# Kernel tuning notes

Measured on AMD Instinct MI355X. Metric: run time of the kernel, lower is better.

The kernel has to match this reference:

```python
import jax, jax.numpy as jnp
import numpy as np

CHAN = 128
IN_CHAN = 3
NB_OUT = 10
K = 2  # maxPoolKer


def affine_grid(theta, H, W):
    # theta: [C,2,3] -> grid [C,H,W,2], torch F.affine_grid align_corners=False
    xs = (2.0 * jnp.arange(W, dtype=jnp.float32) + 1.0) / W - 1.0
    ys = (2.0 * jnp.arange(H, dtype=jnp.float32) + 1.0) / H - 1.0
    gx, gy = jnp.meshgrid(xs, ys)  # [H,W]
    base = jnp.stack([gx, gy, jnp.ones_like(gx)], axis=-1)  # [H,W,3]
    return jnp.einsum('crk,hwk->chwr', theta, base)  # [...,0]=x, [...,1]=y


def grid_sample(img, grid):
    # img [M,H,W], grid [M,H,W,2]; bilinear, zeros padding, align_corners=False
    M, H, W = img.shape
    ix = ((grid[..., 0] + 1.0) * W - 1.0) * 0.5
    iy = ((grid[..., 1] + 1.0) * H - 1.0) * 0.5
    x0 = jnp.floor(ix)
    y0 = jnp.floor(iy)
    wx = ix - x0
    wy = iy - y0

    def tap(xi, yi):
        valid = (xi >= 0) & (xi <= W - 1) & (yi >= 0) & (yi <= H - 1)
        xc = jnp.clip(xi, 0, W - 1).astype(jnp.int32)
        yc = jnp.clip(yi, 0, H - 1).astype(jnp.int32)
        v = jax.vmap(lambda im, y, x: im[y, x])(img, yc, xc)
        return jnp.where(valid, v, 0.0)

    v00 = tap(x0, y0)
    v01 = tap(x0 + 1.0, y0)
    v10 = tap(x0, y0 + 1.0)
    v11 = tap(x0 + 1.0, y0 + 1.0)
    return (1.0 - wy) * ((1.0 - wx) * v00 + wx * v01) + wy * ((1.0 - wx) * v10 + wx * v11)


def geom_layer(x, geo, lin, box):
    # x [B,Ci,H,W]; lin [C,Ci]; geo,box [C,2,3]
    B, Ci, H, W = x.shape
    C = lin.shape[0]
    y = jnp.einsum('ci,bihw->bchw', lin, x)  # channel linear combine
    grid = affine_grid(geo, H, W)            # [C,H,W,2], shared across batch
    samp = jax.vmap(lambda yb: grid_sample(yb, grid))(y)  # [B,C,H,W]
    bgrid = affine_grid(box, H, W)
    boxm = grid_sample(jnp.ones((C, H, W), samp.dtype), bgrid)  # BoxPool mask
    return samp * boxm[None]


def maxpool_g(x, k):
    # MaxPool2d_G: depthwise box-filter conv -> argmax -> gather window from padded x
    B, C, H, W = x.shape
    ch, cw = H // k, W // k
    ker = jnp.ones((1, 1, ch, cw), x.dtype) / (ch + cw)
    xr = x.reshape(B * C, 1, H, W)
    conv = jax.lax.conv_general_dilated(
        xr, ker, (1, 1), [(ch // 2, ch // 2), (cw // 2, cw // 2)])
    conv = conv[:, :, :H, :W].reshape(B, C, H * W)
    argm = jnp.argmax(conv, axis=-1)
    r = argm // H  # original code uses origImgSize[0]; assumes square H==W
    c = argm % W
    padH, padW = H + H // k, W + W // k
    top = padH // 2 - H // 2
    left = padW // 2 - W // 2
    padded = jnp.zeros((B, C, padH, padW), x.dtype).at[:, :, top:top + H, left:left + W].set(x)
    r2 = r + H // (2 * k)
    c2 = c + W // (2 * k)
    ri = r2[..., None] + (jnp.arange(ch) - ch // 2)  # [B,C,ch]
    ci = c2[..., None] + (jnp.arange(cw) - cw // 2)  # [B,C,cw]
    gat = jax.vmap(jax.vmap(lambda p, rr, cc: p[rr[:, None], cc[None, :]]))(padded, ri, ci)
    return gat  # [B,C,ch,cw]


def setup_inputs() -> dict:
    key = jax.random.key(0)
    ks = jax.random.split(key, 12)
    eye = jnp.eye(3, dtype=jnp.float32)[:2]  # [2,3]
    x = jax.random.normal(ks[0], (8, IN_CHAN, 64, 64), dtype=jnp.float32)
    geo0 = eye[None] + 0.1 * jax.random.normal(ks[1], (CHAN, 2, 3), dtype=jnp.float32)
    lin0 = jax.random.uniform(ks[2], (CHAN, IN_CHAN), dtype=jnp.float32)
    box0 = eye[None] + 0.1 * jax.random.normal(ks[3], (CHAN, 2, 3), dtype=jnp.float32)
    geos = eye[None, None] + 0.1 * jax.random.normal(ks[4], (3, CHAN, 2, 3), dtype=jnp.float32)
    lins = jax.random.uniform(ks[5], (3, CHAN, CHAN), dtype=jnp.float32)
    boxes = eye[None, None] + 0.1 * jax.random.normal(ks[6], (3, CHAN, 2, 3), dtype=jnp.float32)
    bound = 1.0 / np.sqrt(CHAN)
    dense_w = jax.random.uniform(ks[7], (NB_OUT, CHAN), dtype=jnp.float32, minval=-bound, maxval=bound)
    dense_b = jax.random.uniform(ks[8], (NB_OUT,), dtype=jnp.float32, minval=-bound, maxval=bound)
    return {"x": x, "geo0": geo0, "lin0": lin0, "box0": box0,
            "geos": geos, "lins": lins, "boxes": boxes,
            "dense_w": dense_w, "dense_b": dense_b}


def reference(x, geo0, lin0, box0, geos, lins, boxes, dense_w, dense_b):
    h = geom_layer(x, geo0, lin0, box0)            # inLay: [8,128,64,64]
    h = geom_layer(h, geos[0], lins[0], boxes[0])  # layer 0
    h = maxpool_g(h, K)                            # layer 1 (maxPoolPos=1): [8,128,32,32]
    h = geom_layer(h, geos[1], lins[1], boxes[1])  # layer 2
    h = geom_layer(h, geos[2], lins[2], boxes[2])  # layer 3
    feat = h
    pooled = feat.mean(axis=-1).mean(axis=-1)      # [B,C]
    out = pooled @ dense_w.T + dense_b             # [B,nbOut]
    return out, feat
```

## Files before the change

### kernel.cpp

```cpp
#include <hip/hip_runtime.h>

#define BB 8
#define CC 128

typedef _Float16 f16x4 __attribute__((ext_vector_type(4)));
typedef float f32x4 __attribute__((ext_vector_type(4)));

__device__ __forceinline__ float sample_pad(const float* __restrict__ pl, int stride,
                                            float WF, float ix, float iy) {
  ix = fminf(fmaxf(ix, -1.0f), WF);
  iy = fminf(fmaxf(iy, -1.0f), WF);
  float x0f = floorf(ix), y0f = floorf(iy);
  float wx = ix - x0f, wy = iy - y0f;
  int xi = (int)x0f + 1, yi = (int)y0f + 1;
  const float* p0 = pl + yi * stride + xi;
  float v00 = p0[0], v01 = p0[1], v10 = p0[stride], v11 = p0[stride + 1];
  return (1.0f - wy) * ((1.0f - wx) * v00 + wx * v01) +
         wy * ((1.0f - wx) * v10 + wx * v11);
}

__device__ __forceinline__ float box_mask(float bix, float biy, float WM1) {
  float bx0 = floorf(bix), by0 = floorf(biy);
  float bwx = bix - bx0, bwy = biy - by0;
  float mx = (((bx0 >= 0.0f) && (bx0 <= WM1)) ? (1.0f - bwx) : 0.0f) +
             (((bx0 >= -1.0f) && (bx0 <= WM1 - 1.0f)) ? bwx : 0.0f);
  float my = (((by0 >= 0.0f) && (by0 <= WM1)) ? (1.0f - bwy) : 0.0f) +
             (((by0 >= -1.0f) && (by0 <= WM1 - 1.0f)) ? bwy : 0.0f);
  return mx * my;
}

__global__ __launch_bounds__(256) void inlay_sample_kernel(
    const float* __restrict__ x, const float* __restrict__ lin,
    const float* __restrict__ geo, const float* __restrict__ box,
    const float* __restrict__ db, float* __restrict__ out,
    float* __restrict__ head) {
  const int H = 64, W = 64, HW = 4096;
  __shared__ float cp[67 * 68];
  int bc = blockIdx.x;
  int c = bc & (CC - 1);
  int b = bc >> 7;
  int tid = threadIdx.x;
  if (bc == 0 && tid < 80) head[tid] = db[tid % 10];
  const float* xb = x + (size_t)b * 3 * HW;

  float w0 = lin[c * 3 + 0], w1 = lin[c * 3 + 1], w2 = lin[c * 3 + 2];

  if (tid < 68) {
    cp[tid] = 0.0f; cp[65 * 68 + tid] = 0.0f; cp[66 * 68 + tid] = 0.0f;
  } else if (tid < 132) {
    int r = tid - 67;
    cp[r * 68 + 0] = 0.0f; cp[r * 68 + 65] = 0.0f; cp[r * 68 + 66] = 0.0f;
  }

#pragma unroll
  for (int k = 0; k < 4; ++k) {
    int i4 = tid + k * 256;
    int base = i4 * 4;
    float4 f0 = *reinterpret_cast<const float4*>(&xb[base]);
    float4 f1 = *reinterpret_cast<const float4*>(&xb[HW + base]);
    float4 f2 = *reinterpret_cast<const float4*>(&xb[2 * HW + base]);
    int h = i4 >> 4, w = (i4 & 15) * 4;
    float* d = &cp[(h + 1) * 68 + w + 1];
    d[0] = w0 * f0.x + w1 * f1.x + w2 * f2.x;
    d[1] = w0 * f0.y + w1 * f1.y + w2 * f2.y;
    d[2] = w0 * f0.z + w1 * f1.z + w2 * f2.z;
    d[3] = w0 * f0.w + w1 * f1.w + w2 * f2.w;
  }
  __syncthreads();

  const float* g = geo + c * 6;
  const float* bx = box + c * 6;
  float g0 = g[0], g1 = g[1], g2 = g[2], g3 = g[3], g4 = g[4], g5 = g[5];
  float b0 = bx[0], b1 = bx[1], b2 = bx[2], b3 = bx[3], b4 = bx[4], b5 = bx[5];
  float* o = out + ((size_t)b * CC + c) * HW;

#pragma unroll
  for (int k = 0; k < 16; ++k) {
    int px = tid + k * 256;
    int h = px >> 6, w = px & 63;
    float xs = (2.0f * w + 1.0f) / W - 1.0f;
    float ys = (2.0f * h + 1.0f) / H - 1.0f;
    float ix = ((g0 * xs + g1 * ys + g2 + 1.0f) * W - 1.0f) * 0.5f;
    float iy = ((g3 * xs + g4 * ys + g5 + 1.0f) * H - 1.0f) * 0.5f;
    float samp = sample_pad(cp, 68, 64.0f, ix, iy);
    float bix = ((b0 * xs + b1 * ys + b2 + 1.0f) * W - 1.0f) * 0.5f;
    float biy = ((b3 * xs + b4 * ys + b5 + 1.0f) * H - 1.0f) * 0.5f;
    o[px] = samp * box_mask(bix, biy, 63.0f);
  }
}

__global__ __launch_bounds__(256) void gemm64_mfma_kernel(
    const float* __restrict__ lin, const float* __restrict__ x,
    float* __restrict__ y) {
  const int Ci = 128, HW = 4096;
  __shared__ unsigned int A_lds[64 * 66];
  __shared__ unsigned int B_lds[64 * 66];
  int b = blockIdx.z;
  int row0 = blockIdx.y * 64, col0 = blockIdx.x * 64;
  const float* xb = x + (size_t)b * Ci * HW;
  float* yb = y + (size_t)b * CC * HW;
  int tid = threadIdx.x;

  {
    int row = tid >> 2, kc = (tid & 3) * 32;
    const float* ap = &lin[(row0 + row) * Ci + kc];
    unsigned int* dst = &A_lds[row * 66 + (kc >> 1)];
#pragma unroll
    for (int i = 0; i < 8; ++i) {
      float4 v = *reinterpret_cast<const float4*>(ap + i * 4);
      union { _Float16 h[2]; unsigned int u; } p0, p1;
      p0.h[0] = (_Float16)v.x; p0.h[1] = (_Float16)v.y;
      p1.h[0] = (_Float16)v.z; p1.h[1] = (_Float16)v.w;
      dst[i * 2] = p0.u; dst[i * 2 + 1] = p1.u;
    }
  }
  {
    int kp = tid >> 2, cg = (tid & 3) * 16;
    const float* b0p = &xb[(size_t)(2 * kp) * HW + col0 + cg];
    const float* b1p = &xb[(size_t)(2 * kp + 1) * HW + col0 + cg];
#pragma unroll
    for (int q = 0; q < 4; ++q) {
      float4 v0 = *reinterpret_cast<const float4*>(b0p + q * 4);
      float4 v1 = *reinterpret_cast<const float4*>(b1p + q * 4);
      float e0[4] = {v0.x, v0.y, v0.z, v0.w};
      float e1[4] = {v1.x, v1.y, v1.z, v1.w};
#pragma unroll
      for (int c = 0; c < 4; ++c) {
        union { _Float16 h[2]; unsigned int u; } p;
        p.h[0] = (_Float16)e0[c]; p.h[1] = (_Float16)e1[c];
        B_lds[(cg + q * 4 + c) * 66 + kp] = p.u;
      }
    }
  }
  __syncthreads();

  int w = tid >> 6, l = tid & 63;
  int lr = l & 15, lq = l >> 4;
  f32x4 acc0 = {0.f, 0.f, 0.f, 0.f};
  f32x4 acc1 = acc0, acc2 = acc0, acc3 = acc0;
  const unsigned int* arow = &A_lds[(w * 16 + lr) * 66 + 2 * lq];
  const unsigned int* bcol = &B_lds[lr * 66 + 2 * lq];
#pragma unroll
  for (int s = 0; s < 8; ++s) {
    f16x4 af = *reinterpret_cast<const f16x4*>(arow + s * 8);
    f16x4 b0 = *reinterpret_cast<const f16x4*>(bcol + 0 * 16 * 66 + s * 8);
    f16x4 b1 = *reinterpret_cast<const f16x4*>(bcol + 1 * 16 * 66 + s * 8);
    f16x4 b2 = *reinterpret_cast<const f16x4*>(bcol + 2 * 16 * 66 + s * 8);
    f16x4 b3 = *reinterpret_cast<const f16x4*>(bcol + 3 * 16 * 66 + s * 8);
    acc0 = __builtin_amdgcn_mfma_f32_16x16x16f16(af, b0, acc0, 0, 0, 0);
    acc1 = __builtin_amdgcn_mfma_f32_16x16x16f16(af, b1, acc1, 0, 0, 0);
    acc2 = __builtin_amdgcn_mfma_f32_16x16x16f16(af, b2, acc2, 0, 0, 0);
    acc3 = __builtin_amdgcn_mfma_f32_16x16x16f16(af, b3, acc3, 0, 0, 0);
  }
#pragma unroll
  for (int i = 0; i < 4; ++i) {
    float* yr = yb + (size_t)(row0 + w * 16 + lq * 4 + i) * HW + col0 + lr;
    yr[0]  = acc0[i];
    yr[16] = acc1[i];
    yr[32] = acc2[i];
    yr[48] = acc3[i];
  }
}

__global__ __launch_bounds__(256) void sampmax_kernel(
    const float* __restrict__ y, const float* __restrict__ geo,
    const float* __restrict__ box, float* __restrict__ out) {
  __shared__ __align__(16) float sp[64 * 68];
  __shared__ __align__(16) float arena[67 * 68];
  __shared__ float wv[4];
  __shared__ int wi[4];
  __shared__ int am_s;
  float* pl = arena;
  float* cb = arena;

  int bc = blockIdx.x;
  int c = bc & (CC - 1);
  int tid = threadIdx.x;

  if (tid < 68) {
    pl[tid] = 0.0f; pl[65 * 68 + tid] = 0.0f; pl[66 * 68 + tid] = 0.0f;
  } else if (tid < 132) {
    int r = tid - 67;
    pl[r * 68 + 0] = 0.0f; pl[r * 68 + 65] = 0.0f; pl[r * 68 + 66] = 0.0f;
  }
  {
    const float* plane = y + (size_t)bc * 4096;
#pragma unroll
    for (int k = 0; k < 4; ++k) {
      int i4 = tid + k * 256;
      float4 f = *reinterpret_cast<const float4*>(&plane[i4 * 4]);
      int h = i4 >> 4, w = (i4 & 15) * 4;
      float* d = &pl[(h + 1) * 68 + w + 1];
      d[0] = f.x; d[1] = f.y; d[2] = f.z; d[3] = f.w;
    }
  }
  __syncthreads();

  {
    const float* g = geo + c * 6;
    const float* bx = box + c * 6;
    float g0 = g[0], g1 = g[1], g2 = g[2], g3 = g[3], g4 = g[4], g5 = g[5];
    float b0 = bx[0], b1 = bx[1], b2 = bx[2], b3 = bx[3], b4 = bx[4], b5 = bx[5];
#pragma unroll
    for (int k = 0; k < 16; ++k) {
      int px = tid + k * 256;
      int h = px >> 6, w = px & 63;
      float xs = (2.0f * w + 1.0f) / 64.0f - 1.0f;
      float ys = (2.0f * h + 1.0f) / 64.0f - 1.0f;
      float ix = ((g0 * xs + g1 * ys + g2 + 1.0f) * 64.0f - 1.0f) * 0.5f;
      float iy = ((g3 * xs + g4 * ys + g5 + 1.0f) * 64.0f - 1.0f) * 0.5f;
      float samp = sample_pad(pl, 68, 64.0f, ix, iy);
      float bix = ((b0 * xs + b1 * ys + b2 + 1.0f) * 64.0f - 1.0f) * 0.5f;
      float biy = ((b3 * xs + b4 * ys + b5 + 1.0f) * 64.0f - 1.0f) * 0.5f;
      sp[h * 68 + w] = samp * box_mask(bix, biy, 63.0f);
    }
  }
  __syncthreads();

  {
    int strip = tid >> 4, w4 = (tid & 15) * 4;
    int h0 = strip * 4;
    float4 a = make_float4(0.f, 0.f, 0.f, 0.f);
    float4 keep0 = a, keep1 = a, keep2 = a;
#pragma unroll
    for (int j = 0; j < 32; ++j) {
      int r = h0 + j - 16;
      bool valid = (r >= 0) && (r < 64);
      int rc = valid ? r : 0;
      float4 f = *reinterpret_cast<const float4*>(&sp[rc * 68 + w4]);
      f.x = valid ? f.x : 0.0f; f.y = valid ? f.y : 0.0f;
      f.z = valid ? f.z : 0.0f; f.w = valid ? f.w : 0.0f;
      if (j == 0) keep0 = f;
      if (j == 1) keep1 = f;
      if (j == 2) keep2 = f;
      a.x += f.x; a.y += f.y; a.z += f.z; a.w += f.w;
    }
    *reinterpret_cast<float4*>(&cb[(h0 + 0) * 68 + w4]) = a;
#pragma unroll
    for (int j = 32; j < 35; ++j) {
      int r = h0 + j - 16;
      bool valid = (r < 64);
      int rc = valid ? r : 0;
      float4 f = *reinterpret_cast<const float4*>(&sp[rc * 68 + w4]);
      f.x = valid ? f.x : 0.0f; f.y = valid ? f.y : 0.0f;
      f.z = valid ? f.z : 0.0f; f.w = valid ? f.w : 0.0f;
      float4 kp = (j == 32) ? keep0 : ((j == 33) ? keep1 : keep2);
      a.x += f.x - kp.x; a.y += f.y - kp.y; a.z += f.z - kp.z; a.w += f.w - kp.w;
      *reinterpret_cast<float4*>(&cb[(h0 + j - 31) * 68 + w4]) = a;
    }
  }
  __syncthreads();

  float best = -3.402823466e+38f;
  int bidx = 0x7fffffff;
#pragma unroll
  for (int hh = 0; hh < 4; ++hh) {
    int h = (tid >> 4) + hh * 16;
    int w4 = (tid & 15) * 4;
    float s0 = 0.f, k0 = 0.f, k1 = 0.f, k2 = 0.f;
#pragma unroll
    for (int q = 0; q < 8; ++q) {
      int u0 = w4 - 16 + 4 * q;
      bool ok = (u0 >= 0) && (u0 <= 60);
      int uc = ok ? u0 : 0;
      float4 f = *reinterpret_cast<const float4*>(&cb[h * 68 + uc]);
      f.x = ok ? f.x : 0.0f; f.y = ok ? f.y : 0.0f;
      f.z = ok ? f.z : 0.0f; f.w = ok ? f.w : 0.0f;
      if (q == 0) { k0 = f.x; k1 = f.y; k2 = f.z; }
      s0 += f.x; s0 += f.y; s0 += f.z; s0 += f.w;
    }
    float ftx = 0.f, fty = 0.f, ftz = 0.f;
    {
      int u0 = w4 + 16;
      bool ok = (u0 <= 60);
      int uc = ok ? u0 : 0;
      float4 f = *reinterpret_cast<const float4*>(&cb[h * 68 + uc]);
      ftx = ok ? f.x : 0.0f; fty = ok ? f.y : 0.0f; ftz = ok ? f.z : 0.0f;
    }
    float s1 = s0 - k0 + ftx;
    float s2 = s1 - k1 + fty;
    float s3 = s2 - k2 + ftz;
    float sv[4] = {s0, s1, s2, s3};
#pragma unroll
    for (int d = 0; d < 4; ++d) {
      int i = (h << 6) + w4 + d;
      if (sv[d] > best) { best = sv[d]; bidx = i; }
    }
  }
#pragma unroll
  for (int off = 32; off > 0; off >>= 1) {
    float v2 = __shfl_down(best, off);
    int i2 = __shfl_down(bidx, off);
    if (v2 > best || (v2 == best && i2 < bidx)) { best = v2; bidx = i2; }
  }
  if ((tid & 63) == 0) { wv[tid >> 6] = best; wi[tid >> 6] = bidx; }
  __syncthreads();
  if (tid == 0) {
    float bv = wv[0]; int bi = wi[0];
#pragma unroll
    for (int k = 1; k < 4; ++k)
      if (wv[k] > bv || (wv[k] == bv && wi[k] < bi)) { bv = wv[k]; bi = wi[k]; }
    am_s = bi;
  }
  __syncthreads();

  int am = am_s;
  int r = am >> 6, cx = am & 63;
  float* o = out + (size_t)bc * 1024;
#pragma unroll
  for (int k = 0; k < 4; ++k) {
    int idx = tid + k * 256;
    int oi = idx >> 5, oj = idx & 31;
    int rr = r + oi - 16, cj = cx + oj - 16;
    bool v = (rr >= 0) && (rr < 64) && (cj >= 0) && (cj < 64);
    int rrc = v ? rr : 0, cjc = v ? cj : 0;
    o[idx] = v ? sp[rrc * 68 + cjc] : 0.0f;
  }
}

__global__ __launch_bounds__(256) void gemm32_kernel(
    const float* __restrict__ lin, const float* __restrict__ x,
    float* __restrict__ y) {
  const int Ci = 128, HW = 1024;
  __shared__ __align__(16) float As[16][36];
  __shared__ __align__(16) float Bs[16][64];
  int b = blockIdx.z;
  const float* xb = x + (size_t)b * Ci * HW;
  float* yb = y + (size_t)b * CC * HW;
  int tid = threadIdx.x;
  int tx = tid & 15, ty = tid >> 4;
  int row0 = blockIdx.y * 32;
  int col0 = blockIdx.x * 64;
  int m = tid >> 2, kq = (tid & 3) * 4;
  int kk = tid >> 4, n4 = (tid & 15) * 4;
  float acc[2][4] = {};
  float4 ra = make_float4(0.f, 0.f, 0.f, 0.f);
  if (tid < 128) ra = *reinterpret_cast<const float4*>(&lin[(row0 + m) * Ci + kq]);
  float4 rb = *reinterpret_cast<const float4*>(&xb[(size_t)kk * HW + col0 + n4]);
  for (int k0 = 0; k0 < 128; k0 += 16) {
    __syncthreads();
    if (tid < 128) { As[kq + 0][m] = ra.x; As[kq + 1][m] = ra.y; As[kq + 2][m] = ra.z; As[kq + 3][m] = ra.w; }
    *reinterpret_cast<float4*>(&Bs[kk][n4]) = rb;
    __syncthreads();
    if (k0 + 16 < 128) {
      if (tid < 128) ra = *reinterpret_cast<const float4*>(&lin[(row0 + m) * Ci + k0 + 16 + kq]);
      rb = *reinterpret_cast<const float4*>(&xb[(size_t)(k0 + 16 + kk) * HW + col0 + n4]);
    }
#pragma unroll
    for (int kki = 0; kki < 16; ++kki) {
      float a0 = As[kki][ty * 2], a1 = As[kki][ty * 2 + 1];
      float4 b4 = *reinterpret_cast<const float4*>(&Bs[kki][tx * 4]);
      acc[0][0] += a0 * b4.x; acc[0][1] += a0 * b4.y; acc[0][2] += a0 * b4.z; acc[0][3] += a0 * b4.w;
      acc[1][0] += a1 * b4.x; acc[1][1] += a1 * b4.y; acc[1][2] += a1 * b4.z; acc[1][3] += a1 * b4.w;
    }
  }
#pragma unroll
  for (int i = 0; i < 2; i++) {
    float* yr = yb + (size_t)(row0 + ty * 2 + i) * HW + col0 + tx * 4;
    *reinterpret_cast<float4*>(yr) = make_float4(acc[i][0], acc[i][1], acc[i][2], acc[i][3]);
  }
}

template <bool POOL>
__global__ __launch_bounds__(256) void sample32_kernel(
    const float* __restrict__ y, const float* __restrict__ geo,
    const float* __restrict__ box, float* __restrict__ out,
    const float* __restrict__ dw, float* __restrict__ head) {
  const int W = 32, HW = 1024;
  __shared__ float pl[35 * 36];
  __shared__ float wred[4];
  int bc = blockIdx.x;
  int c = bc & (CC - 1);
  int b = bc >> 7;
  int tid = threadIdx.x;

  if (tid < 36) {
    pl[tid] = 0.0f; pl[33 * 36 + tid] = 0.0f; pl[34 * 36 + tid] = 0.0f;
  } else if (tid < 68) {
    int r = tid - 35;
    pl[r * 36 + 0] = 0.0f; pl[r * 36 + 33] = 0.0f; pl[r * 36 + 34] = 0.0f; pl[r * 36 + 35] = 0.0f;
  }
  {
    const float* plane = y + (size_t)bc * HW;
    float4 f = *reinterpret_cast<const float4*>(&plane[tid * 4]);
    int h = tid >> 3, w = (tid & 7) * 4;
    float* d = &pl[(h + 1) * 36 + w + 1];
    d[0] = f.x; d[1] = f.y; d[2] = f.z; d[3] = f.w;
  }
  __syncthreads();

  const float* g = geo + c * 6;
  const float* bxp = box + c * 6;
  float g0 = g[0], g1 = g[1], g2 = g[2], g3 = g[3], g4 = g[4], g5 = g[5];
  float b0 = bxp[0], b1 = bxp[1], b2 = bxp[2], b3 = bxp[3], b4 = bxp[4], b5 = bxp[5];
  float* o = out + (size_t)bc * HW;
  float psum = 0.f;
#pragma unroll
  for (int k = 0; k < 4; ++k) {
    int px = tid + k * 256;
    int h = px >> 5, w = px & 31;
    float xs = (2.0f * w + 1.0f) / W - 1.0f;
    float ys = (2.0f * h + 1.0f) / W - 1.0f;
    float ix = ((g0 * xs + g1 * ys + g2 + 1.0f) * W - 1.0f) * 0.5f;
    float iy = ((g3 * xs + g4 * ys + g5 + 1.0f) * W - 1.0f) * 0.5f;
    float samp = sample_pad(pl, 36, 32.0f, ix, iy);
    float bix = ((b0 * xs + b1 * ys + b2 + 1.0f) * W - 1.0f) * 0.5f;
    float biy = ((b3 * xs + b4 * ys + b5 + 1.0f) * W - 1.0f) * 0.5f;
    float res = samp * box_mask(bix, biy, 31.0f);
    o[px] = res;
    if (POOL) psum += res;
  }
  if (POOL) {
    int lane = tid & 63, wid = tid >> 6;
    float r = psum;
#pragma unroll
    for (int off = 32; off > 0; off >>= 1) r += __shfl_down(r, off);
    if (lane == 0) wred[wid] = r;
    __syncthreads();
    if (tid < 10) {
      float t = (wred[0] + wred[1] + wred[2] + wred[3]) * (1.0f / 1024.0f);
      atomicAdd(&head[b * 10 + tid], t * dw[tid * 128 + c]);
    }
  }
}

extern "C" void kernel_launch(void* const* d_in, const int* in_sizes, int n_in,
                              void* d_out, int out_size, void* d_ws, size_t ws_size,
                              hipStream_t stream) {
  const float* x     = (const float*)d_in[0];
  const float* geo0  = (const float*)d_in[1];
  const float* lin0  = (const float*)d_in[2];
  const float* box0  = (const float*)d_in[3];
  const float* geos  = (const float*)d_in[4];
  const float* lins  = (const float*)d_in[5];
  const float* boxes = (const float*)d_in[6];
  const float* dw    = (const float*)d_in[7];
  const float* db    = (const float*)d_in[8];

  float* out  = (float*)d_out;
  float* feat = out + 80;
  float* ws   = (float*)d_ws;
  float* ws0  = ws;
  float* ws1  = ws + 4194304;
  float* ws2  = ws + 8388608;

  inlay_sample_kernel<<<dim3(BB * CC), 256, 0, stream>>>(x, lin0, geo0, box0, db, ws1, out);
  gemm64_mfma_kernel<<<dim3(64, 2, BB), 256, 0, stream>>>(lins, ws1, ws0);
  sampmax_kernel<<<dim3(BB * CC), 256, 0, stream>>>(ws0, geos, boxes, ws1);
  gemm32_kernel<<<dim3(16, 4, BB), 256, 0, stream>>>(lins + 16384, ws1, ws2);
  sample32_kernel<false><<<dim3(BB * CC), 256, 0, stream>>>(ws2, geos + 768, boxes + 768, ws0, nullptr, nullptr);
  gemm32_kernel<<<dim3(16, 4, BB), 256, 0, stream>>>(lins + 32768, ws0, ws2);
  sample32_kernel<true><<<dim3(BB * CC), 256, 0, stream>>>(ws2, geos + 1536, boxes + 1536, feat, dw, out);
}
```

Before: 146.6 us.

## Fuse 32x32 layer channel-mix GEMM with grid sampling using fp16 MFMA

Replaces the separate fp32 GEMM and sampling kernels for the two 32x32 layers with one fused kernel. Each block computes 16 output channels for all 1024 pixels using fp16 MFMA, writes the results into padded LDS planes, and then does the bilinear sample, box mask and optional pooled head in place. This removes two launches and the global round trip of the intermediate tensor. In exchange, only 64 blocks are launched, each block re-reads the full input batch slice, and fp16 rounding of the inputs and weights reduces precision.

Result: slower. 153.9 us (+5.0%).

```diff
diff --git a/kernel.cpp b/kernel.cpp
--- a/kernel.cpp
+++ b/kernel.cpp
@@ -318,108 +318,131 @@
   }
 }
 
-__global__ __launch_bounds__(256) void gemm32_kernel(
+template <bool POOL>
+__global__ __launch_bounds__(512) void fusedgs32_kernel(
     const float* __restrict__ lin, const float* __restrict__ x,
-    float* __restrict__ y) {
-  const int Ci = 128, HW = 1024;
-  __shared__ __align__(16) float As[16][36];
-  __shared__ __align__(16) float Bs[16][64];
-  int b = blockIdx.z;
-  const float* xb = x + (size_t)b * Ci * HW;
-  float* yb = y + (size_t)b * CC * HW;
+    const float* __restrict__ geo, const float* __restrict__ box,
+    float* __restrict__ out, const float* __restrict__ dw,
+    float* __restrict__ head) {
+  __shared__ __align__(16) float arena[20160];
+  __shared__ __align__(16) unsigned int A_lds[16 * 66];
+  __shared__ float wred[16];
+  unsigned int* Bw = reinterpret_cast<unsigned int*>(arena);
+  float* planes = arena;
+
+  int c0 = blockIdx.x * 16;
+  int b = blockIdx.y;
   int tid = threadIdx.x;
-  int tx = tid & 15, ty = tid >> 4;
-  int row0 = blockIdx.y * 32;
-  int col0 = blockIdx.x * 64;
-  int m = tid >> 2, kq = (tid & 3) * 4;
-  int kk = tid >> 4, n4 = (tid & 15) * 4;
-  float acc[2][4] = {};
-  float4 ra = make_float4(0.f, 0.f, 0.f, 0.f);
-  if (tid < 128) ra = *reinterpret_cast<const float4*>(&lin[(row0 + m) * Ci + kq]);
-  float4 rb = *reinterpret_cast<const float4*>(&xb[(size_t)kk * HW + col0 + n4]);
-  for (int k0 = 0; k0 < 128; k0 += 16) {
+  const float* xb = x + (size_t)b * 128 * 1024;
+
+  if (tid < 256) {
+    int row = tid >> 4, kg = tid & 15;
+    const float* ap = &lin[(c0 + row) * 128 + kg * 8];
+    float4 v0 = *reinterpret_cast<const float4*>(ap);
+    float4 v1 = *reinterpret_cast<const float4*>(ap + 4);
+    unsigned int* dst = &A_lds[row * 66 + kg * 4];
+    union { _Float16 h[2]; unsigned int u; } p;
+    p.h[0] = (_Float16)v0.x; p.h[1] = (_Float16)v0.y; dst[0] = p.u;
+    p.h[0] = (_Float16)v0.z; p.h[1] = (_Float16)v0.w; dst[1] = p.u;
+    p.h[0] = (_Float16)v1.x; p.h[1] = (_Float16)v1.y; dst[2] = p.u;
+    p.h[0] = (_Float16)v1.z; p.h[1] = (_Float16)v1.w; dst[3] = p.u;
+  }
+
+  int w = tid >> 6, l = tid & 63;
+  int lr = l & 15, lq = l >> 4;
+  f32x4 acc[8];
+#pragma unroll
+  for (int j = 0; j < 8; ++j) acc[j] = (f32x4){0.f, 0.f, 0.f, 0.f};
+
+  const unsigned int* arow = &A_lds[lr * 66 + 2 * lq];
+
+  for (int kc = 0; kc < 4; ++kc) {
+    if (kc) __syncthreads();
+    {
+      int kpl = tid >> 5;
+      int cg = tid & 31;
+      const float* r0 = xb + (size_t)(kc * 32 + 2 * kpl) * 1024;
+      const float* r1 = r0 + 1024;
+#pragma unroll
+      for (int q = 0; q < 8; ++q) {
+        int col = q * 128 + cg * 4;
+        float4 v0 = *reinterpret_cast<const float4*>(r0 + col);
+        float4 v1 = *reinterpret_cast<const float4*>(r1 + col);
+        float e0[4] = {v0.x, v0.y, v0.z, v0.w};
+        float e1[4] = {v1.x, v1.y, v1.z, v1.w};
+#pragma unroll
+        for (int e = 0; e < 4; ++e) {
+          union { _Float16 h[2]; unsigned int u; } p;
+          p.h[0] = (_Float16)e0[e]; p.h[1] = (_Float16)e1[e];
+          Bw[(col + e) * 18 + kpl] = p.u;
+        }
+      }
+    }
     __syncthreads();
-    if (tid < 128) { As[kq + 0][m] = ra.x; As[kq + 1][m] = ra.y; As[kq + 2][m] = ra.z; As[kq + 3][m] = ra.w; }
-    *reinterpret_cast<float4*>(&Bs[kk][n4]) = rb;
-    __syncthreads();
-    if (k0 + 16 < 128) {
-      if (tid < 128) ra = *reinterpret_cast<const float4*>(&lin[(row0 + m) * Ci + k0 + 16 + kq]);
-      rb = *reinterpret_cast<const float4*>(&xb[(size_t)(k0 + 16 + kk) * HW + col0 + n4]);
-    }
-#pragma unroll
-    for (int kki = 0; kki < 16; ++kki) {
-      float a0 = As[kki][ty * 2], a1 = As[kki][ty * 2 + 1];
-      float4 b4 = *reinterpret_cast<const float4*>(&Bs[kki][tx * 4]);
-      acc[0][0] += a0 * b4.x; acc[0][1] += a0 * b4.y; acc[0][2] += a0 * b4.z; acc[0][3] += a0 * b4.w;
-      acc[1][0] += a1 * b4.x; acc[1][1] += a1 * b4.y; acc[1][2] += a1 * b4.z; acc[1][3] += a1 * b4.w;
-    }
-  }
-#pragma unroll
-  for (int i = 0; i < 2; i++) {
-    float* yr = yb + (size_t)(row0 + ty * 2 + i) * HW + col0 + tx * 4;
-    *reinterpret_cast<float4*>(yr) = make_float4(acc[i][0], acc[i][1], acc[i][2], acc[i][3]);
-  }
-}
-
-template <bool POOL>
-__global__ __launch_bounds__(256) void sample32_kernel(
-    const float* __restrict__ y, const float* __restrict__ geo,
-    const float* __restrict__ box, float* __restrict__ out,
-    const float* __restrict__ dw, float* __restrict__ head) {
-  const int W = 32, HW = 1024;
-  __shared__ float pl[35 * 36];
-  __shared__ float wred[4];
-  int bc = blockIdx.x;
-  int c = bc & (CC - 1);
-  int b = bc >> 7;
-  int tid = threadIdx.x;
-
-  if (tid < 36) {
-    pl[tid] = 0.0f; pl[33 * 36 + tid] = 0.0f; pl[34 * 36 + tid] = 0.0f;
-  } else if (tid < 68) {
-    int r = tid - 35;
-    pl[r * 36 + 0] = 0.0f; pl[r * 36 + 33] = 0.0f; pl[r * 36 + 34] = 0.0f; pl[r * 36 + 35] = 0.0f;
-  }
-  {
-    const float* plane = y + (size_t)bc * HW;
-    float4 f = *reinterpret_cast<const float4*>(&plane[tid * 4]);
-    int h = tid >> 3, w = (tid & 7) * 4;
-    float* d = &pl[(h + 1) * 36 + w + 1];
-    d[0] = f.x; d[1] = f.y; d[2] = f.z; d[3] = f.w;
-  }
-  __syncthreads();
-
-  const float* g = geo + c * 6;
-  const float* bxp = box + c * 6;
-  float g0 = g[0], g1 = g[1], g2 = g[2], g3 = g[3], g4 = g[4], g5 = g[5];
-  float b0 = bxp[0], b1 = bxp[1], b2 = bxp[2], b3 = bxp[3], b4 = bxp[4], b5 = bxp[5];
-  float* o = out + (size_t)bc * HW;
-  float psum = 0.f;
-#pragma unroll
-  for (int k = 0; k < 4; ++k) {
-    int px = tid + k * 256;
-    int h = px >> 5, w = px & 31;
-    float xs = (2.0f * w + 1.0f) / W - 1.0f;
-    float ys = (2.0f * h + 1.0f) / W - 1.0f;
-    float ix = ((g0 * xs + g1 * ys + g2 + 1.0f) * W - 1.0f) * 0.5f;
-    float iy = ((g3 * xs + g4 * ys + g5 + 1.0f) * W - 1.0f) * 0.5f;
-    float samp = sample_pad(pl, 36, 32.0f, ix, iy);
-    float bix = ((b0 * xs + b1 * ys + b2 + 1.0f) * W - 1.0f) * 0.5f;
-    float biy = ((b3 * xs + b4 * ys + b5 + 1.0f) * W - 1.0f) * 0.5f;
-    float res = samp * box_mask(bix, biy, 31.0f);
-    o[px] = res;
-    if (POOL) psum += res;
+#pragma unroll
+    for (int s = 0; s < 2; ++s) {
+      f16x4 af = *reinterpret_cast<const f16x4*>(arow + kc * 16 + s * 8);
+#pragma unroll
+      for (int j = 0; j < 8; ++j) {
+        int colbase = (w * 8 + j) * 16 + lr;
+        f16x4 bf = *reinterpret_cast<const f16x4*>(&Bw[colbase * 18 + s * 8 + 2 * lq]);
+        acc[j] = __builtin_amdgcn_mfma_f32_16x16x16f16(af, bf, acc[j], 0, 0, 0);
+      }
+    }
+  }
+  __syncthreads();
+
+  for (int i = tid; i < 20160; i += 512) planes[i] = 0.0f;
+  __syncthreads();
+#pragma unroll
+  for (int j = 0; j < 8; ++j) {
+    int px = (w * 8 + j) * 16 + lr;
+    int h = px >> 5, wc = px & 31;
+    float* base = &planes[(h + 1) * 36 + wc + 1];
+#pragma unroll
+    for (int i = 0; i < 4; ++i) {
+      base[(4 * lq + i) * 1260] = acc[j][i];
+    }
+  }
+  __syncthreads();
+
+  {
+    int ch = tid >> 5, lane32 = tid & 31;
+    int c = c0 + ch;
+    const float* g = geo + c * 6;
+    const float* bp = box + c * 6;
+    float g0 = g[0], g1 = g[1], g2 = g[2], g3 = g[3], g4 = g[4], g5 = g[5];
+    float b0 = bp[0], b1 = bp[1], b2 = bp[2], b3 = bp[3], b4 = bp[4], b5 = bp[5];
+    const float* pl = &planes[ch * 1260];
+    float* o = out + ((size_t)b * CC + c) * 1024;
+    float psum = 0.f;
+    float xs = (2.0f * lane32 + 1.0f) / 32.0f - 1.0f;
+#pragma unroll
+    for (int k = 0; k < 32; ++k) {
+      float ys = (2.0f * k + 1.0f) / 32.0f - 1.0f;
+      float ix = ((g0 * xs + g1 * ys + g2 + 1.0f) * 32.0f - 1.0f) * 0.5f;
+      float iy = ((g3 * xs + g4 * ys + g5 + 1.0f) * 32.0f - 1.0f) * 0.5f;
+      float samp = sample_pad(pl, 36, 32.0f, ix, iy);
+      float bix = ((b0 * xs + b1 * ys + b2 + 1.0f) * 32.0f - 1.0f) * 0.5f;
+      float biy = ((b3 * xs + b4 * ys + b5 + 1.0f) * 32.0f - 1.0f) * 0.5f;
+      float res = samp * box_mask(bix, biy, 31.0f);
+      o[k * 32 + lane32] = res;
+      if (POOL) psum += res;
+    }
+    if (POOL) {
+#pragma unroll
+      for (int m = 16; m >= 1; m >>= 1) psum += __shfl_xor(psum, m);
+      if (lane32 == 0) wred[ch] = psum;
+    }
   }
   if (POOL) {
-    int lane = tid & 63, wid = tid >> 6;
-    float r = psum;
-#pragma unroll
-    for (int off = 32; off > 0; off >>= 1) r += __shfl_down(r, off);
-    if (lane == 0) wred[wid] = r;
     __syncthreads();
     if (tid < 10) {
-      float t = (wred[0] + wred[1] + wred[2] + wred[3]) * (1.0f / 1024.0f);
-      atomicAdd(&head[b * 10 + tid], t * dw[tid * 128 + c]);
+      float s = 0.f;
+#pragma unroll
+      for (int ch = 0; ch < 16; ++ch)
+        s += wred[ch] * (1.0f / 1024.0f) * dw[tid * 128 + c0 + ch];
+      atomicAdd(&head[b * 10 + tid], s);
     }
   }
 }
@@ -442,13 +465,12 @@
   float* ws   = (float*)d_ws;
   float* ws0  = ws;
   float* ws1  = ws + 4194304;
-  float* ws2  = ws + 8388608;
 
   inlay_sample_kernel<<<dim3(BB * CC), 256, 0, stream>>>(x, lin0, geo0, box0, db, ws1, out);
   gemm64_mfma_kernel<<<dim3(64, 2, BB), 256, 0, stream>>>(lins, ws1, ws0);
   sampmax_kernel<<<dim3(BB * CC), 256, 0, stream>>>(ws0, geos, boxes, ws1);
-  gemm32_kernel<<<dim3(16, 4, BB), 256, 0, stream>>>(lins + 16384, ws1, ws2);
-  sample32_kernel<false><<<dim3(BB * CC), 256, 0, stream>>>(ws2, geos + 768, boxes + 768, ws0, nullptr, nullptr);
-  gemm32_kernel<<<dim3(16, 4, BB), 256, 0, stream>>>(lins + 32768, ws0, ws2);
-  sample32_kernel<true><<<dim3(BB * CC), 256, 0, stream>>>(ws2, geos + 1536, boxes + 1536, feat, dw, out);
-}
+  fusedgs32_kernel<false><<<dim3(8, 8), 512, 0, stream>>>(
+      lins + 16384, ws1, geos + 768, boxes + 768, ws0, nullptr, nullptr);
+  fusedgs32_kernel<true><<<dim3(8, 8), 512, 0, stream>>>(
+      lins + 32768, ws0, geos + 1536, boxes + 1536, feat, dw, out);
+}
```
